# Optimization experiments

Hardware: AMD Instinct MI355X
Metric: run time of the kernel (lower is better)

The kernel has to match this reference:

```python
import jax, jax.numpy as jnp
import numpy as np
from jax import lax

TS = 1.0  # sampling time


def setup_inputs() -> dict:
    key = jax.random.key(0)
    k1, k2, k3, k4 = jax.random.split(key, 4)
    q, m, n_x, n_u, h = 8192, 2048, 2, 1, 64
    x0 = jax.random.normal(k1, (q, n_x), dtype=jnp.float32)
    u = jax.random.normal(k2, (m, q, n_u), dtype=jnp.float32)
    # small neural state-space model: f(x, u) = tanh([x, u] @ W1 + b1) @ W2 + b2
    W1 = jax.random.normal(k3, (n_x + n_u, h), dtype=jnp.float32) * (1.0 / np.sqrt(n_x + n_u))
    b1 = jnp.zeros((h,), dtype=jnp.float32)
    W2 = jax.random.normal(k4, (h, n_x), dtype=jnp.float32) * 0.01
    b2 = jnp.zeros((n_x,), dtype=jnp.float32)
    return {"x0": x0, "u": u, "W1": W1, "b1": b1, "W2": W2, "b2": b2}


def reference(x0, u, W1, b1, W2, b2):
    ts = TS
    dt2 = ts / 2.0

    def f(x, u_step):
        # x: (q, n_x), u_step: (q, n_u) -> dx: (q, n_x)
        h = jnp.tanh(jnp.concatenate([x, u_step], axis=-1) @ W1 + b1)
        return h @ W2 + b2

    def step(x, u_step):
        k1 = f(x, u_step)
        k2 = f(x + dt2 * k1, u_step)
        k3 = f(x + dt2 * k2, u_step)
        k4 = f(x + ts * k3, u_step)
        x_new = x + (ts / 6.0) * (k1 + 2.0 * k2 + 2.0 * k3 + k4)
        return x_new, x  # output is state BEFORE update (matches torch loop)

    _, X_sim = lax.scan(step, x0, u)
    return X_sim  # (m, q, n_x)
```

## Files before the change

### kernel.cpp

```cpp
#include <hip/hip_runtime.h>

typedef float v2f __attribute__((ext_vector_type(2)));

#define QN 8192
#define MN 2048
#define HN 64
#define LPT 16
#define UPL 4

template <int CTRL>
__device__ __forceinline__ float dpp_add(float v) {
    int m = __builtin_amdgcn_update_dpp(__float_as_int(v), __float_as_int(v),
                                        CTRL, 0xf, 0xf, true);
    return v + __int_as_float(m);
}
#define DPP_QUAD_XOR1 0xB1
#define DPP_QUAD_XOR2 0x4E
#define DPP_HALF_MIRR 0x141
#define DPP_ROW_MIRR  0x140

__device__ __forceinline__ v2f vfma(v2f a, v2f b, v2f c) {
    return __builtin_elementwise_fma(a, b, c);
}

__global__ __launch_bounds__(256, 2) void rk4_nss_kernel(
    const float* __restrict__ x0p,
    const float* __restrict__ up,
    const float* __restrict__ W1,
    const float* __restrict__ b1,
    const float* __restrict__ W2,
    const float* __restrict__ b2,
    float* __restrict__ out)
{
    const int tid  = blockIdx.x * 256 + threadIdx.x;
    const int lane = threadIdx.x & (LPT - 1);
    const int traj = tid >> 4;

    const float SC = 2.8853900817779268f;
    const float CL = 27.0f;

    v2f W10[2], W11[2], W12[2], BS[2];
    float w20n[UPL], w21n[UPL];
#pragma unroll
    for (int k = 0; k < UPL; ++k) {
        const int j = lane + k * LPT;
        W10[k >> 1][k & 1] = W1[j] * SC;
        W11[k >> 1][k & 1] = W1[HN + j] * SC;
        W12[k >> 1][k & 1] = W1[2 * HN + j] * SC;
        BS[k >> 1][k & 1]  = b1[j] * SC;
        w20n[k] = -2.0f * W2[2 * j];
        w21n[k] = -2.0f * W2[2 * j + 1];
    }
    float c0 = b2[0], c1 = b2[1];
    for (int j = 0; j < HN; ++j) {
        c0 += W2[2 * j];
        c1 += W2[2 * j + 1];
    }
    const float c0h = 0.5f * c0, c1h = 0.5f * c1;

    float xa = x0p[2 * traj];
    float xb = x0p[2 * traj + 1];

    float2* op = reinterpret_cast<float2*>(out) + traj;
    const bool writer = (lane == 0);

    v2f PB[2];

    auto feval = [&](float ia, float ib, float& p0o, float& p1o) {
        v2f IA = {ia, ia};
        v2f IB = {ib, ib};
        v2f PRE0 = vfma(W10[0], IA, vfma(W11[0], IB, PB[0]));
        v2f PRE1 = vfma(W10[1], IA, vfma(W11[1], IB, PB[1]));
        float den0 = __builtin_amdgcn_exp2f(__builtin_amdgcn_fmed3f(PRE0.x, -CL, CL)) + 1.0f;
        float den1 = __builtin_amdgcn_exp2f(__builtin_amdgcn_fmed3f(PRE0.y, -CL, CL)) + 1.0f;
        float den2 = __builtin_amdgcn_exp2f(__builtin_amdgcn_fmed3f(PRE1.x, -CL, CL)) + 1.0f;
        float den3 = __builtin_amdgcn_exp2f(__builtin_amdgcn_fmed3f(PRE1.y, -CL, CL)) + 1.0f;
        float d01 = den0 * den1;
        float d23 = den2 * den3;
        float r01 = __builtin_amdgcn_rcpf(d01);
        float r23 = __builtin_amdgcn_rcpf(d23);
        float inv0 = r01 * den1;
        float inv1 = r01 * den0;
        float inv2 = r23 * den3;
        float inv3 = r23 * den2;

        float p0 = fmaf(inv0, w20n[0],
                   fmaf(inv1, w20n[1],
                   fmaf(inv2, w20n[2], inv3 * w20n[3])));
        float p1 = fmaf(inv0, w21n[0],
                   fmaf(inv1, w21n[1],
                   fmaf(inv2, w21n[2], inv3 * w21n[3])));

        p0 = dpp_add<DPP_QUAD_XOR1>(p0);  p1 = dpp_add<DPP_QUAD_XOR1>(p1);
        p0 = dpp_add<DPP_QUAD_XOR2>(p0);  p1 = dpp_add<DPP_QUAD_XOR2>(p1);
        p0 = dpp_add<DPP_HALF_MIRR>(p0);  p1 = dpp_add<DPP_HALF_MIRR>(p1);
        p0 = dpp_add<DPP_ROW_MIRR>(p0);   p1 = dpp_add<DPP_ROW_MIRR>(p1);
        p0o = p0;
        p1o = p1;
    };

    auto step = [&](float u, int ) {
        v2f UU = {u, u};
        PB[0] = vfma(W12[0], UU, BS[0]);
        PB[1] = vfma(W12[1], UU, BS[1]);

        const float xha = xa + c0h, xhb = xb + c1h;
        const float xca = xa + c0,  xcb = xb + c1;

        float p1a, p1b, p2a, p2b, p3a, p3b, p4a, p4b;
        feval(xa, xb, p1a, p1b);
        feval(fmaf(0.5f, p1a, xha), fmaf(0.5f, p1b, xhb), p2a, p2b);
        feval(fmaf(0.5f, p2a, xha), fmaf(0.5f, p2b, xhb), p3a, p3b);
        feval(xca + p3a, xcb + p3b, p4a, p4b);

        float ta = p2a + p3a, sa = p1a + p4a;
        xa = fmaf(1.0f / 6.0f, fmaf(2.0f, ta, sa), xca);
        float tb = p2b + p3b, sb = p1b + p4b;
        xb = fmaf(1.0f / 6.0f, fmaf(2.0f, tb, sb), xcb);
    };

    float u0 = up[traj];
    float u1 = up[QN + traj];

    for (int t = 0; t < MN; t += 2) {
        const float u2 = (t + 2 < MN) ? up[(t + 2) * QN + traj] : 0.0f;
        const float u3 = (t + 3 < MN) ? up[(t + 3) * QN + traj] : 0.0f;

        if (writer) *op = make_float2(xa, xb);
        op += QN;
        step(u0, t);

        if (writer) *op = make_float2(xa, xb);
        op += QN;
        step(u1, t + 1);

        u0 = u2;
        u1 = u3;
    }
}

extern "C" void kernel_launch(void* const* d_in, const int* in_sizes, int n_in,
                              void* d_out, int out_size, void* d_ws, size_t ws_size,
                              hipStream_t stream) {
    const float* x0 = (const float*)d_in[0];
    const float* u  = (const float*)d_in[1];
    const float* W1 = (const float*)d_in[2];
    const float* b1 = (const float*)d_in[3];
    const float* W2 = (const float*)d_in[4];
    const float* b2 = (const float*)d_in[5];
    float* out = (float*)d_out;

    const int threads = 256;
    const int blocks  = (QN * LPT) / threads;
    rk4_nss_kernel<<<blocks, threads, 0, stream>>>(x0, u, W1, b1, W2, b2, out);
}
```

Before: 1.826 ms.

## Process two trajectories per 16-lane group to raise instruction-level parallelism

Each 16-lane group now integrates two independent trajectories at once, interleaving their feval chains so exp/rcp/DPP latencies of one hide behind the other. The grid is halved, so there are half as many waves overall, and launch bounds drop to one block per SIMD pair to allow more registers. Input u is loaded as float2 for the trajectory pair, and two lanes write the outputs. This trades wave-level parallelism for ILP inside each wave, and the higher register use may lower occupancy.

New measurement: 1.893 ms. +3.6%, slower.

```diff
diff --git a/kernel.cpp b/kernel.cpp
--- a/kernel.cpp
+++ b/kernel.cpp
@@ -23,7 +23,7 @@
     return __builtin_elementwise_fma(a, b, c);
 }
 
-__global__ __launch_bounds__(256, 2) void rk4_nss_kernel(
+__global__ __launch_bounds__(256, 1) void rk4_nss_kernel(
     const float* __restrict__ x0p,
     const float* __restrict__ up,
     const float* __restrict__ W1,
@@ -32,9 +32,10 @@
     const float* __restrict__ b2,
     float* __restrict__ out)
 {
-    const int tid  = blockIdx.x * 256 + threadIdx.x;
-    const int lane = threadIdx.x & (LPT - 1);
-    const int traj = tid >> 4;
+    const int tid   = blockIdx.x * 256 + threadIdx.x;
+    const int glane = threadIdx.x & (LPT - 1);
+    const int gid   = tid >> 4;
+    const int trajA = 2 * gid;
 
     const float SC = 2.8853900817779268f;
     const float CL = 27.0f;
@@ -43,7 +44,7 @@
     float w20n[UPL], w21n[UPL];
 #pragma unroll
     for (int k = 0; k < UPL; ++k) {
-        const int j = lane + k * LPT;
+        const int j = glane + k * LPT;
         W10[k >> 1][k & 1] = W1[j] * SC;
         W11[k >> 1][k & 1] = W1[HN + j] * SC;
         W12[k >> 1][k & 1] = W1[2 * HN + j] * SC;
@@ -58,84 +59,116 @@
     }
     const float c0h = 0.5f * c0, c1h = 0.5f * c1;
 
-    float xa = x0p[2 * traj];
-    float xb = x0p[2 * traj + 1];
+    float xaA = x0p[2 * trajA],     xbA = x0p[2 * trajA + 1];
+    float xaB = x0p[2 * trajA + 2], xbB = x0p[2 * trajA + 3];
 
-    float2* op = reinterpret_cast<float2*>(out) + traj;
-    const bool writer = (lane == 0);
+    float2* op = reinterpret_cast<float2*>(out) + trajA;
+    const bool writer = (glane < 2);
+    const bool isA    = (glane == 0);
 
-    v2f PB[2];
+    v2f PBA[2], PBB[2];
 
-    auto feval = [&](float ia, float ib, float& p0o, float& p1o) {
-        v2f IA = {ia, ia};
-        v2f IB = {ib, ib};
-        v2f PRE0 = vfma(W10[0], IA, vfma(W11[0], IB, PB[0]));
-        v2f PRE1 = vfma(W10[1], IA, vfma(W11[1], IB, PB[1]));
-        float den0 = __builtin_amdgcn_exp2f(__builtin_amdgcn_fmed3f(PRE0.x, -CL, CL)) + 1.0f;
-        float den1 = __builtin_amdgcn_exp2f(__builtin_amdgcn_fmed3f(PRE0.y, -CL, CL)) + 1.0f;
-        float den2 = __builtin_amdgcn_exp2f(__builtin_amdgcn_fmed3f(PRE1.x, -CL, CL)) + 1.0f;
-        float den3 = __builtin_amdgcn_exp2f(__builtin_amdgcn_fmed3f(PRE1.y, -CL, CL)) + 1.0f;
-        float d01 = den0 * den1;
-        float d23 = den2 * den3;
-        float r01 = __builtin_amdgcn_rcpf(d01);
-        float r23 = __builtin_amdgcn_rcpf(d23);
-        float inv0 = r01 * den1;
-        float inv1 = r01 * den0;
-        float inv2 = r23 * den3;
-        float inv3 = r23 * den2;
+    auto feval2 = [&](float iaA_, float ibA_, float iaB_, float ibB_,
+                      float& p0A, float& p1A, float& p0B, float& p1B) {
+        v2f IAA = {iaA_, iaA_}, IBA = {ibA_, ibA_};
+        v2f IAB = {iaB_, iaB_}, IBB = {ibB_, ibB_};
+        v2f PA0 = vfma(W10[0], IAA, vfma(W11[0], IBA, PBA[0]));
+        v2f PA1 = vfma(W10[1], IAA, vfma(W11[1], IBA, PBA[1]));
+        v2f PB0 = vfma(W10[0], IAB, vfma(W11[0], IBB, PBB[0]));
+        v2f PB1 = vfma(W10[1], IAB, vfma(W11[1], IBB, PBB[1]));
 
-        float p0 = fmaf(inv0, w20n[0],
-                   fmaf(inv1, w20n[1],
-                   fmaf(inv2, w20n[2], inv3 * w20n[3])));
-        float p1 = fmaf(inv0, w21n[0],
-                   fmaf(inv1, w21n[1],
-                   fmaf(inv2, w21n[2], inv3 * w21n[3])));
+        float dA0 = __builtin_amdgcn_exp2f(__builtin_amdgcn_fmed3f(PA0.x, -CL, CL)) + 1.0f;
+        float dA1 = __builtin_amdgcn_exp2f(__builtin_amdgcn_fmed3f(PA0.y, -CL, CL)) + 1.0f;
+        float dA2 = __builtin_amdgcn_exp2f(__builtin_amdgcn_fmed3f(PA1.x, -CL, CL)) + 1.0f;
+        float dA3 = __builtin_amdgcn_exp2f(__builtin_amdgcn_fmed3f(PA1.y, -CL, CL)) + 1.0f;
+        float dB0 = __builtin_amdgcn_exp2f(__builtin_amdgcn_fmed3f(PB0.x, -CL, CL)) + 1.0f;
+        float dB1 = __builtin_amdgcn_exp2f(__builtin_amdgcn_fmed3f(PB0.y, -CL, CL)) + 1.0f;
+        float dB2 = __builtin_amdgcn_exp2f(__builtin_amdgcn_fmed3f(PB1.x, -CL, CL)) + 1.0f;
+        float dB3 = __builtin_amdgcn_exp2f(__builtin_amdgcn_fmed3f(PB1.y, -CL, CL)) + 1.0f;
 
-        p0 = dpp_add<DPP_QUAD_XOR1>(p0);  p1 = dpp_add<DPP_QUAD_XOR1>(p1);
-        p0 = dpp_add<DPP_QUAD_XOR2>(p0);  p1 = dpp_add<DPP_QUAD_XOR2>(p1);
-        p0 = dpp_add<DPP_HALF_MIRR>(p0);  p1 = dpp_add<DPP_HALF_MIRR>(p1);
-        p0 = dpp_add<DPP_ROW_MIRR>(p0);   p1 = dpp_add<DPP_ROW_MIRR>(p1);
-        p0o = p0;
-        p1o = p1;
+        float rA01 = __builtin_amdgcn_rcpf(dA0 * dA1);
+        float rA23 = __builtin_amdgcn_rcpf(dA2 * dA3);
+        float rB01 = __builtin_amdgcn_rcpf(dB0 * dB1);
+        float rB23 = __builtin_amdgcn_rcpf(dB2 * dB3);
+        float iA0 = rA01 * dA1, iA1 = rA01 * dA0;
+        float iA2 = rA23 * dA3, iA3 = rA23 * dA2;
+        float iB0 = rB01 * dB1, iB1 = rB01 * dB0;
+        float iB2 = rB23 * dB3, iB3 = rB23 * dB2;
+
+        float q0A = fmaf(iA0, w20n[0], fmaf(iA1, w20n[1],
+                    fmaf(iA2, w20n[2], iA3 * w20n[3])));
+        float q1A = fmaf(iA0, w21n[0], fmaf(iA1, w21n[1],
+                    fmaf(iA2, w21n[2], iA3 * w21n[3])));
+        float q0B = fmaf(iB0, w20n[0], fmaf(iB1, w20n[1],
+                    fmaf(iB2, w20n[2], iB3 * w20n[3])));
+        float q1B = fmaf(iB0, w21n[0], fmaf(iB1, w21n[1],
+                    fmaf(iB2, w21n[2], iB3 * w21n[3])));
+
+        q0A = dpp_add<DPP_QUAD_XOR1>(q0A);  q1A = dpp_add<DPP_QUAD_XOR1>(q1A);
+        q0B = dpp_add<DPP_QUAD_XOR1>(q0B);  q1B = dpp_add<DPP_QUAD_XOR1>(q1B);
+        q0A = dpp_add<DPP_QUAD_XOR2>(q0A);  q1A = dpp_add<DPP_QUAD_XOR2>(q1A);
+        q0B = dpp_add<DPP_QUAD_XOR2>(q0B);  q1B = dpp_add<DPP_QUAD_XOR2>(q1B);
+        q0A = dpp_add<DPP_HALF_MIRR>(q0A);  q1A = dpp_add<DPP_HALF_MIRR>(q1A);
+        q0B = dpp_add<DPP_HALF_MIRR>(q0B);  q1B = dpp_add<DPP_HALF_MIRR>(q1B);
+        q0A = dpp_add<DPP_ROW_MIRR>(q0A);   q1A = dpp_add<DPP_ROW_MIRR>(q1A);
+        q0B = dpp_add<DPP_ROW_MIRR>(q0B);   q1B = dpp_add<DPP_ROW_MIRR>(q1B);
+        p0A = q0A; p1A = q1A; p0B = q0B; p1B = q1B;
     };
 
-    auto step = [&](float u, int ) {
-        v2f UU = {u, u};
-        PB[0] = vfma(W12[0], UU, BS[0]);
-        PB[1] = vfma(W12[1], UU, BS[1]);
+    auto step2 = [&](float uA, float uB) {
+        v2f UA = {uA, uA}, UB = {uB, uB};
+        PBA[0] = vfma(W12[0], UA, BS[0]);
+        PBA[1] = vfma(W12[1], UA, BS[1]);
+        PBB[0] = vfma(W12[0], UB, BS[0]);
+        PBB[1] = vfma(W12[1], UB, BS[1]);
 
-        const float xha = xa + c0h, xhb = xb + c1h;
-        const float xca = xa + c0,  xcb = xb + c1;
+        const float xhaA = xaA + c0h, xhbA = xbA + c1h;
+        const float xcaA = xaA + c0,  xcbA = xbA + c1;
+        const float xhaB = xaB + c0h, xhbB = xbB + c1h;
+        const float xcaB = xaB + c0,  xcbB = xbB + c1;
 
-        float p1a, p1b, p2a, p2b, p3a, p3b, p4a, p4b;
-        feval(xa, xb, p1a, p1b);
-        feval(fmaf(0.5f, p1a, xha), fmaf(0.5f, p1b, xhb), p2a, p2b);
-        feval(fmaf(0.5f, p2a, xha), fmaf(0.5f, p2b, xhb), p3a, p3b);
-        feval(xca + p3a, xcb + p3b, p4a, p4b);
+        float p1aA, p1bA, p2aA, p2bA, p3aA, p3bA, p4aA, p4bA;
+        float p1aB, p1bB, p2aB, p2bB, p3aB, p3bB, p4aB, p4bB;
+        feval2(xaA, xbA, xaB, xbB, p1aA, p1bA, p1aB, p1bB);
+        feval2(fmaf(0.5f, p1aA, xhaA), fmaf(0.5f, p1bA, xhbA),
+               fmaf(0.5f, p1aB, xhaB), fmaf(0.5f, p1bB, xhbB),
+               p2aA, p2bA, p2aB, p2bB);
+        feval2(fmaf(0.5f, p2aA, xhaA), fmaf(0.5f, p2bA, xhbA),
+               fmaf(0.5f, p2aB, xhaB), fmaf(0.5f, p2bB, xhbB),
+               p3aA, p3bA, p3aB, p3bB);
+        feval2(xcaA + p3aA, xcbA + p3bA, xcaB + p3aB, xcbB + p3bB,
+               p4aA, p4bA, p4aB, p4bB);
 
-        float ta = p2a + p3a, sa = p1a + p4a;
-        xa = fmaf(1.0f / 6.0f, fmaf(2.0f, ta, sa), xca);
-        float tb = p2b + p3b, sb = p1b + p4b;
-        xb = fmaf(1.0f / 6.0f, fmaf(2.0f, tb, sb), xcb);
+        xaA = fmaf(1.0f / 6.0f, fmaf(2.0f, p2aA + p3aA, p1aA + p4aA), xcaA);
+        xbA = fmaf(1.0f / 6.0f, fmaf(2.0f, p2bA + p3bA, p1bA + p4bA), xcbA);
+        xaB = fmaf(1.0f / 6.0f, fmaf(2.0f, p2aB + p3aB, p1aB + p4aB), xcaB);
+        xbB = fmaf(1.0f / 6.0f, fmaf(2.0f, p2bB + p3bB, p1bB + p4bB), xcbB);
     };
 
-    float u0 = up[traj];
-    float u1 = up[QN + traj];
+    const float2* upv = reinterpret_cast<const float2*>(up) + gid;
+    float2 u01 = upv[0];
+    float2 u23 = upv[QN / 2];
 
     for (int t = 0; t < MN; t += 2) {
-        const float u2 = (t + 2 < MN) ? up[(t + 2) * QN + traj] : 0.0f;
-        const float u3 = (t + 3 < MN) ? up[(t + 3) * QN + traj] : 0.0f;
+        const float2 un0 = (t + 2 < MN) ? upv[(t + 2) * (QN / 2)]
+                                        : make_float2(0.0f, 0.0f);
+        const float2 un1 = (t + 3 < MN) ? upv[(t + 3) * (QN / 2)]
+                                        : make_float2(0.0f, 0.0f);
 
-        if (writer) *op = make_float2(xa, xb);
+        if (writer) {
+            op[glane] = isA ? make_float2(xaA, xbA) : make_float2(xaB, xbB);
+        }
         op += QN;
-        step(u0, t);
+        step2(u01.x, u01.y);
 
-        if (writer) *op = make_float2(xa, xb);
+        if (writer) {
+            op[glane] = isA ? make_float2(xaA, xbA) : make_float2(xaB, xbB);
+        }
         op += QN;
-        step(u1, t + 1);
+        step2(u23.x, u23.y);
 
-        u0 = u2;
-        u1 = u3;
+        u01 = un0;
+        u23 = un1;
     }
 }
 
@@ -151,6 +184,6 @@
     float* out = (float*)d_out;
 
     const int threads = 256;
-    const int blocks  = (QN * LPT) / threads;
+    const int blocks  = (QN / 2 * LPT) / threads;
     rk4_nss_kernel<<<blocks, threads, 0, stream>>>(x0, u, W1, b1, W2, b2, out);
 }
```

## Spread each trajectory over 32 lanes with permlane32 cross-row reduction

Applied to the files above, without the earlier changes.

Reassigns work so each trajectory uses 32 lanes, with two hidden units per lane instead of four, and adds a permlane32 swap to finish the hidden-layer reduction across half-waves. This halves per-lane exp/rcp work on the serial RK4 dependency chain and doubles the wave count, with launch bounds raised for higher occupancy. The cost is an extra cross-lane reduction stage and more total instructions issued per trajectory, which may compete for SIMD issue slots.

Result: slower. 2.445 ms (+33.9%).

```diff
diff --git a/kernel.cpp b/kernel.cpp
--- a/kernel.cpp
+++ b/kernel.cpp
@@ -1,12 +1,12 @@
 #include <hip/hip_runtime.h>
 
 typedef float v2f __attribute__((ext_vector_type(2)));
+typedef int   v2i __attribute__((ext_vector_type(2)));
 
 #define QN 8192
 #define MN 2048
 #define HN 64
-#define LPT 16
-#define UPL 4
+#define UPL 2
 
 template <int CTRL>
 __device__ __forceinline__ float dpp_add(float v) {
@@ -19,11 +19,17 @@
 #define DPP_HALF_MIRR 0x141
 #define DPP_ROW_MIRR  0x140
 
+__device__ __forceinline__ float xor32_add(float p) {
+    v2i pr = __builtin_amdgcn_permlane32_swap(__float_as_int(p), __float_as_int(p),
+                                              false, false);
+    return __int_as_float(pr.x) + __int_as_float(pr.y);
+}
+
 __device__ __forceinline__ v2f vfma(v2f a, v2f b, v2f c) {
     return __builtin_elementwise_fma(a, b, c);
 }
 
-__global__ __launch_bounds__(256, 2) void rk4_nss_kernel(
+__global__ __launch_bounds__(256, 4) void rk4_nss_kernel(
     const float* __restrict__ x0p,
     const float* __restrict__ up,
     const float* __restrict__ W1,
@@ -32,22 +38,25 @@
     const float* __restrict__ b2,
     float* __restrict__ out)
 {
-    const int tid  = blockIdx.x * 256 + threadIdx.x;
-    const int lane = threadIdx.x & (LPT - 1);
-    const int traj = tid >> 4;
+    const int tid    = blockIdx.x * 256 + threadIdx.x;
+    const int lane64 = threadIdx.x & 63;
+    const int wid    = tid >> 6;
+    const int group  = (lane64 >> 4) & 1;
+    const int traj   = 2 * wid + group;
+    const int s      = (lane64 & 15) + ((lane64 & 32) >> 1);
 
     const float SC = 2.8853900817779268f;
     const float CL = 27.0f;
 
-    v2f W10[2], W11[2], W12[2], BS[2];
+    v2f W10, W11, W12, BS;
     float w20n[UPL], w21n[UPL];
 #pragma unroll
     for (int k = 0; k < UPL; ++k) {
-        const int j = lane + k * LPT;
-        W10[k >> 1][k & 1] = W1[j] * SC;
-        W11[k >> 1][k & 1] = W1[HN + j] * SC;
-        W12[k >> 1][k & 1] = W1[2 * HN + j] * SC;
-        BS[k >> 1][k & 1]  = b1[j] * SC;
+        const int j = s + 32 * k;
+        W10[k] = W1[j] * SC;
+        W11[k] = W1[HN + j] * SC;
+        W12[k] = W1[2 * HN + j] * SC;
+        BS[k]  = b1[j] * SC;
         w20n[k] = -2.0f * W2[2 * j];
         w21n[k] = -2.0f * W2[2 * j + 1];
     }
@@ -61,48 +70,36 @@
     float xa = x0p[2 * traj];
     float xb = x0p[2 * traj + 1];
 
-    float2* op = reinterpret_cast<float2*>(out) + traj;
-    const bool writer = (lane == 0);
+    float2* op = reinterpret_cast<float2*>(out) + 2 * wid;
+    const bool writer = ((lane64 & 47) == 0);
 
-    v2f PB[2];
+    v2f PB;
 
     auto feval = [&](float ia, float ib, float& p0o, float& p1o) {
         v2f IA = {ia, ia};
         v2f IB = {ib, ib};
-        v2f PRE0 = vfma(W10[0], IA, vfma(W11[0], IB, PB[0]));
-        v2f PRE1 = vfma(W10[1], IA, vfma(W11[1], IB, PB[1]));
-        float den0 = __builtin_amdgcn_exp2f(__builtin_amdgcn_fmed3f(PRE0.x, -CL, CL)) + 1.0f;
-        float den1 = __builtin_amdgcn_exp2f(__builtin_amdgcn_fmed3f(PRE0.y, -CL, CL)) + 1.0f;
-        float den2 = __builtin_amdgcn_exp2f(__builtin_amdgcn_fmed3f(PRE1.x, -CL, CL)) + 1.0f;
-        float den3 = __builtin_amdgcn_exp2f(__builtin_amdgcn_fmed3f(PRE1.y, -CL, CL)) + 1.0f;
-        float d01 = den0 * den1;
-        float d23 = den2 * den3;
-        float r01 = __builtin_amdgcn_rcpf(d01);
-        float r23 = __builtin_amdgcn_rcpf(d23);
-        float inv0 = r01 * den1;
-        float inv1 = r01 * den0;
-        float inv2 = r23 * den3;
-        float inv3 = r23 * den2;
+        v2f PRE = vfma(W10, IA, vfma(W11, IB, PB));
+        float den0 = __builtin_amdgcn_exp2f(__builtin_amdgcn_fmed3f(PRE.x, -CL, CL)) + 1.0f;
+        float den1 = __builtin_amdgcn_exp2f(__builtin_amdgcn_fmed3f(PRE.y, -CL, CL)) + 1.0f;
+        float r    = __builtin_amdgcn_rcpf(den0 * den1);
+        float inv0 = r * den1;
+        float inv1 = r * den0;
 
-        float p0 = fmaf(inv0, w20n[0],
-                   fmaf(inv1, w20n[1],
-                   fmaf(inv2, w20n[2], inv3 * w20n[3])));
-        float p1 = fmaf(inv0, w21n[0],
-                   fmaf(inv1, w21n[1],
-                   fmaf(inv2, w21n[2], inv3 * w21n[3])));
+        float p0 = fmaf(inv0, w20n[0], inv1 * w20n[1]);
+        float p1 = fmaf(inv0, w21n[0], inv1 * w21n[1]);
 
         p0 = dpp_add<DPP_QUAD_XOR1>(p0);  p1 = dpp_add<DPP_QUAD_XOR1>(p1);
         p0 = dpp_add<DPP_QUAD_XOR2>(p0);  p1 = dpp_add<DPP_QUAD_XOR2>(p1);
         p0 = dpp_add<DPP_HALF_MIRR>(p0);  p1 = dpp_add<DPP_HALF_MIRR>(p1);
         p0 = dpp_add<DPP_ROW_MIRR>(p0);   p1 = dpp_add<DPP_ROW_MIRR>(p1);
+        p0 = xor32_add(p0);               p1 = xor32_add(p1);
         p0o = p0;
         p1o = p1;
     };
 
-    auto step = [&](float u, int ) {
+    auto step = [&](float u) {
         v2f UU = {u, u};
-        PB[0] = vfma(W12[0], UU, BS[0]);
-        PB[1] = vfma(W12[1], UU, BS[1]);
+        PB = vfma(W12, UU, BS);
 
         const float xha = xa + c0h, xhb = xb + c1h;
         const float xca = xa + c0,  xcb = xb + c1;
@@ -126,13 +123,13 @@
         const float u2 = (t + 2 < MN) ? up[(t + 2) * QN + traj] : 0.0f;
         const float u3 = (t + 3 < MN) ? up[(t + 3) * QN + traj] : 0.0f;
 
-        if (writer) *op = make_float2(xa, xb);
+        if (writer) op[group] = make_float2(xa, xb);
         op += QN;
-        step(u0, t);
+        step(u0);
 
-        if (writer) *op = make_float2(xa, xb);
+        if (writer) op[group] = make_float2(xa, xb);
         op += QN;
-        step(u1, t + 1);
+        step(u1);
 
         u0 = u2;
         u1 = u3;
@@ -151,6 +148,6 @@
     float* out = (float*)d_out;
 
     const int threads = 256;
-    const int blocks  = (QN * LPT) / threads;
+    const int blocks  = (QN / 2 * 64) / threads;
     rk4_nss_kernel<<<blocks, threads, 0, stream>>>(x0, u, W1, b1, W2, b2, out);
 }
```
